# Kernel optimization log

Measured on AMD Instinct MI355X. Metric: run time of the kernel, lower is better.

## Reference

```python
import jax, jax.numpy as jnp
import numpy as np


def setup_inputs() -> dict:
    key = jax.random.key(0)
    k1, k2, k3 = jax.random.split(key, 3)
    N1, N2, P, D = 4, 8, 1024, 128  # P = PH*PW = 32*32 (512px / 16 patch)
    feats = jax.random.normal(k1, (N1, P, D), dtype=jnp.float32)
    nfeats = jax.random.normal(k2, (N2, P, D), dtype=jnp.float32)
    background_masks = jax.random.uniform(k3, (N1, P), dtype=jnp.float32)
    return {"feats": feats, "nfeats": nfeats, "background_masks": background_masks,
            "PH": 32, "PW": 32, "H": 512, "W": 512}


def reference(feats, nfeats, background_masks, PH, PW, H, W):
    # L2-normalize patch embeddings (as in `f / f.norm(dim=-1, keepdim=True)`)
    f = feats / jnp.linalg.norm(feats, axis=-1, keepdims=True)    # [N1,P,D]
    g = nfeats / jnp.linalg.norm(nfeats, axis=-1, keepdims=True)  # [N2,Q,D]
    # Euclidean cdist of unit vectors: d^2 = 2 - 2*dot (clamped at 0)
    dot = jnp.einsum('npd,mqd->nmpq', f, g)                        # [N1,N2,P,Q]
    dist = jnp.sqrt(jnp.maximum(2.0 - 2.0 * dot, 0.0)) / 2.0      # cdist/2, permuted
    # min over normal patches Q -> per-query-patch nearest-neighbor distance
    scores_patch = dist.min(axis=-1)                               # [N1,N2,P]
    scores_patch = scores_patch * background_masks[:, None, :]
    # image score: max over query patches, mean over normal images
    scores = scores_patch.max(axis=-1).mean(axis=-1)               # [N1]
    # pixel map: mean over normal images, reshape to patch grid, bilinear upsample
    sp = scores_patch.mean(axis=1).reshape(-1, PH, PW)             # [N1,PH,PW]
    scores_pixel = jax.image.resize(sp, (sp.shape[0], H, W), method='bilinear')
    return scores, scores_pixel
```

## Files before the change

### kernel.cpp

```cpp
#include <hip/hip_runtime.h>

typedef __attribute__((ext_vector_type(8))) short short8;
typedef __attribute__((ext_vector_type(4))) float f32x4;

typedef const __attribute__((address_space(1))) unsigned int glb_u32;
typedef __attribute__((address_space(3))) unsigned int lds_u32;

static __device__ inline unsigned short f2bf(float x) {
    unsigned int u = __float_as_uint(x);
    u = (u + 0x7FFFu + ((u >> 16) & 1u)) >> 16;
    return (unsigned short)u;
}

__global__ __launch_bounds__(256) void knorm(const float* __restrict__ feats,
                                             const float* __restrict__ nfeats,
                                             unsigned short* __restrict__ fb,
                                             unsigned short* __restrict__ gb) {
    int row = blockIdx.x * 4 + (threadIdx.x >> 6);
    int lane = threadIdx.x & 63;
    const float* src;
    unsigned short* dst;
    if (row < 4096) { src = feats + row * 128;           dst = fb + row * 128; }
    else            { src = nfeats + (row - 4096) * 128; dst = gb + (row - 4096) * 128; }
    float2 v = ((const float2*)src)[lane];
    float ss = v.x * v.x + v.y * v.y;
    #pragma unroll
    for (int d = 32; d; d >>= 1) ss += __shfl_xor(ss, d);
    float inv = 1.0f / sqrtf(ss);
    ushort2 o;
    o.x = f2bf(v.x * inv);
    o.y = f2bf(v.y * inv);
    ((ushort2*)dst)[lane] = o;
}

__global__ __launch_bounds__(512, 4) void kscore(const unsigned short* __restrict__ fb,
                                                 const unsigned short* __restrict__ gb,
                                                 float* __restrict__ sp_part) {
    __shared__ unsigned short gtile[2][64 * 128];
    const int tid = threadIdx.x;
    const int lane = tid & 63;
    const int wave = tid >> 6;
    const int l15 = lane & 15, lhi = lane >> 4;
    const int n = blockIdx.z;
    const int m = blockIdx.y >> 2, qc = blockIdx.y & 3;
    const int pbase = blockIdx.x * 256 + wave * 32;

    short8 a[2][4];
    #pragma unroll
    for (int pg = 0; pg < 2; pg++) {
        const unsigned short* arow = fb + (size_t)(n * 1024 + pbase + pg * 16 + l15) * 128;
        #pragma unroll
        for (int kk = 0; kk < 4; kk++)
            a[pg][kk] = *(const short8*)(arow + kk * 32 + lhi * 8);
    }

    f32x4 mx[2];
    #pragma unroll
    for (int i = 0; i < 4; i++) { mx[0][i] = -1e30f; mx[1][i] = -1e30f; }

    const unsigned short* gBase = gb + ((size_t)m * 1024 + qc * 256) * 128;

    auto stage = [&](int buf, int qb) {
        #pragma unroll
        for (int c = tid; c < 1024; c += 512) {
            int r = c >> 4, s = c & 15;
            int scol = s ^ (r & 7);
            __builtin_amdgcn_global_load_lds(
                (glb_u32*)(gBase + (size_t)(qb + r) * 128 + scol * 8),
                (lds_u32*)((char*)gtile[buf] + c * 16), 16, 0, 0);
        }
    };

    stage(0, 0);
    __syncthreads();
    int buf = 0;
    #pragma unroll
    for (int it = 0; it < 4; it++) {
        if (it < 3) stage(buf ^ 1, (it + 1) * 64);
        const char* tp = (const char*)gtile[buf];
        #pragma unroll
        for (int qt = 0; qt < 4; qt++) {
            int r = qt * 16 + l15;
            int rowoff = r * 256;
            int swz = (r & 7) << 4;
            f32x4 acc0 = {0.f, 0.f, 0.f, 0.f};
            f32x4 acc1 = {0.f, 0.f, 0.f, 0.f};
            #pragma unroll
            for (int kk = 0; kk < 4; kk++) {
                short8 b = *(const short8*)(tp + ((rowoff + kk * 64 + lhi * 16) ^ swz));
                acc0 = __builtin_amdgcn_mfma_f32_16x16x32_bf16(a[0][kk], b, acc0, 0, 0, 0);
                acc1 = __builtin_amdgcn_mfma_f32_16x16x32_bf16(a[1][kk], b, acc1, 0, 0, 0);
            }
            #pragma unroll
            for (int i = 0; i < 4; i++) {
                mx[0][i] = fmaxf(mx[0][i], acc0[i]);
                mx[1][i] = fmaxf(mx[1][i], acc1[i]);
            }
        }
        __syncthreads();
        buf ^= 1;
    }

    #pragma unroll
    for (int pg = 0; pg < 2; pg++)
        #pragma unroll
        for (int i = 0; i < 4; i++) {
            float v = mx[pg][i];
            v = fmaxf(v, __shfl_xor(v, 1));
            v = fmaxf(v, __shfl_xor(v, 2));
            v = fmaxf(v, __shfl_xor(v, 4));
            v = fmaxf(v, __shfl_xor(v, 8));
            mx[pg][i] = v;
        }
    if (l15 == 0) {
        float* dst = sp_part + ((size_t)(n * 8 + m) * 4 + qc) * 1024;
        #pragma unroll
        for (int pg = 0; pg < 2; pg++)
            #pragma unroll
            for (int i = 0; i < 4; i++)
                dst[pbase + pg * 16 + lhi * 4 + i] = mx[pg][i];
    }
}

__global__ __launch_bounds__(256) void kreduce(const float* __restrict__ sp_part,
                                               const float* __restrict__ mask,
                                               float* __restrict__ sp_mean,
                                               float* __restrict__ scores) {
    int n = blockIdx.x, t = threadIdx.x;
    __shared__ float smax[4];
    float sums[4] = {0.f, 0.f, 0.f, 0.f};
    float scoresum = 0.f;
    for (int m = 0; m < 8; m++) {
        const float* base = sp_part + (size_t)(n * 8 + m) * 4 * 1024;
        float lm = -1e30f;
        #pragma unroll
        for (int i = 0; i < 4; i++) {
            int p = i * 256 + t;
            float dot = fmaxf(fmaxf(base[p], base[1024 + p]),
                              fmaxf(base[2048 + p], base[3072 + p]));
            float d = sqrtf(fmaxf(2.0f - 2.0f * dot, 0.0f)) * 0.5f * mask[n * 1024 + p];
            sums[i] += d;
            lm = fmaxf(lm, d);
        }
        #pragma unroll
        for (int d = 32; d; d >>= 1) lm = fmaxf(lm, __shfl_xor(lm, d));
        if ((t & 63) == 0) smax[t >> 6] = lm;
        __syncthreads();
        if (t == 0) scoresum += fmaxf(fmaxf(smax[0], smax[1]), fmaxf(smax[2], smax[3]));
        __syncthreads();
    }
    if (t == 0) scores[n] = scoresum * 0.125f;
    #pragma unroll
    for (int i = 0; i < 4; i++) sp_mean[n * 1024 + i * 256 + t] = sums[i] * 0.125f;
}

__global__ __launch_bounds__(256) void kupsample(const float* __restrict__ sp_mean,
                                                 float* __restrict__ outp) {
    int n = blockIdx.y;
    int idx = blockIdx.x * 256 + threadIdx.x;
    int y = idx >> 9, x = idx & 511;
    float fy = (y + 0.5f) * 0.0625f - 0.5f;
    float fx = (x + 0.5f) * 0.0625f - 0.5f;
    float yf = floorf(fy), xf = floorf(fx);
    float ty = fy - yf, tx = fx - xf;
    int y0 = (int)yf, x0 = (int)xf;
    int y0c = min(max(y0, 0), 31), y1c = min(max(y0 + 1, 0), 31);
    int x0c = min(max(x0, 0), 31), x1c = min(max(x0 + 1, 0), 31);
    const float* s = sp_mean + n * 1024;
    float v00 = s[y0c * 32 + x0c], v01 = s[y0c * 32 + x1c];
    float v10 = s[y1c * 32 + x0c], v11 = s[y1c * 32 + x1c];
    float v0 = v00 + tx * (v01 - v00);
    float v1 = v10 + tx * (v11 - v10);
    outp[(size_t)n * 262144 + idx] = v0 + ty * (v1 - v0);
}

extern "C" void kernel_launch(void* const* d_in, const int* in_sizes, int n_in,
                              void* d_out, int out_size, void* d_ws, size_t ws_size,
                              hipStream_t stream) {
    const float* feats = (const float*)d_in[0];
    const float* nfeats = (const float*)d_in[1];
    const float* mask = (const float*)d_in[2];
    float* out = (float*)d_out;

    unsigned short* fb = (unsigned short*)d_ws;
    unsigned short* gb = fb + 4096 * 128;
    float* sp_part = (float*)((char*)d_ws + 3u * 1024u * 1024u);
    float* sp_mean = sp_part + 4 * 8 * 4 * 1024;

    knorm<<<3072, 256, 0, stream>>>(feats, nfeats, fb, gb);
    kscore<<<dim3(4, 32, 4), 512, 0, stream>>>(fb, gb, sp_part);
    kreduce<<<4, 256, 0, stream>>>(sp_part, mask, sp_mean, out);
    kupsample<<<dim3(1024, 4), 256, 0, stream>>>(sp_mean, out + 4);
}
```

Before: 32.76 us.

## Retile score kernel and fuse reduction with bilinear upsample

```diff
diff --git a/kernel.cpp b/kernel.cpp
--- a/kernel.cpp
+++ b/kernel.cpp
@@ -33,36 +33,38 @@
     ((ushort2*)dst)[lane] = o;
 }
 
-__global__ __launch_bounds__(512, 4) void kscore(const unsigned short* __restrict__ fb,
+__global__ __launch_bounds__(256, 4) void kscore(const unsigned short* __restrict__ fb,
                                                  const unsigned short* __restrict__ gb,
                                                  float* __restrict__ sp_part) {
-    __shared__ unsigned short gtile[2][64 * 128];
+    __shared__ unsigned short gtile[2][32 * 128];
     const int tid = threadIdx.x;
     const int lane = tid & 63;
     const int wave = tid >> 6;
     const int l15 = lane & 15, lhi = lane >> 4;
     const int n = blockIdx.z;
-    const int m = blockIdx.y >> 2, qc = blockIdx.y & 3;
-    const int pbase = blockIdx.x * 256 + wave * 32;
-
-    short8 a[2][4];
-    #pragma unroll
-    for (int pg = 0; pg < 2; pg++) {
+    const int m = blockIdx.y >> 3, qc = blockIdx.y & 7;
+    const int pbase = blockIdx.x * 256 + wave * 64;
+
+    short8 a[4][4];
+    #pragma unroll
+    for (int pg = 0; pg < 4; pg++) {
         const unsigned short* arow = fb + (size_t)(n * 1024 + pbase + pg * 16 + l15) * 128;
         #pragma unroll
         for (int kk = 0; kk < 4; kk++)
             a[pg][kk] = *(const short8*)(arow + kk * 32 + lhi * 8);
     }
 
-    f32x4 mx[2];
-    #pragma unroll
-    for (int i = 0; i < 4; i++) { mx[0][i] = -1e30f; mx[1][i] = -1e30f; }
-
-    const unsigned short* gBase = gb + ((size_t)m * 1024 + qc * 256) * 128;
+    f32x4 mx[4];
+    #pragma unroll
+    for (int pg = 0; pg < 4; pg++)
+        #pragma unroll
+        for (int i = 0; i < 4; i++) mx[pg][i] = -1e30f;
+
+    const unsigned short* gBase = gb + ((size_t)m * 1024 + qc * 128) * 128;
 
     auto stage = [&](int buf, int qb) {
         #pragma unroll
-        for (int c = tid; c < 1024; c += 512) {
+        for (int c = tid; c < 512; c += 256) {
             int r = c >> 4, s = c & 15;
             int scol = s ^ (r & 7);
             __builtin_amdgcn_global_load_lds(
@@ -72,37 +74,43 @@
     };
 
     stage(0, 0);
-    __syncthreads();
-    int buf = 0;
-    #pragma unroll
-    for (int it = 0; it < 4; it++) {
-        if (it < 3) stage(buf ^ 1, (it + 1) * 64);
-        const char* tp = (const char*)gtile[buf];
-        #pragma unroll
-        for (int qt = 0; qt < 4; qt++) {
+    stage(1, 32);
+    #pragma unroll
+    for (int t = 0; t < 4; t++) {
+        if (t < 3) asm volatile("s_waitcnt vmcnt(2)" ::: "memory");
+        else       asm volatile("s_waitcnt vmcnt(0)" ::: "memory");
+        __builtin_amdgcn_s_barrier();
+        __builtin_amdgcn_sched_barrier(0);
+        const char* tp = (const char*)gtile[t & 1];
+        #pragma unroll
+        for (int qt = 0; qt < 2; qt++) {
             int r = qt * 16 + l15;
             int rowoff = r * 256;
             int swz = (r & 7) << 4;
-            f32x4 acc0 = {0.f, 0.f, 0.f, 0.f};
-            f32x4 acc1 = {0.f, 0.f, 0.f, 0.f};
+            f32x4 acc[4];
+            #pragma unroll
+            for (int pg = 0; pg < 4; pg++)
+                #pragma unroll
+                for (int i = 0; i < 4; i++) acc[pg][i] = 0.f;
             #pragma unroll
             for (int kk = 0; kk < 4; kk++) {
                 short8 b = *(const short8*)(tp + ((rowoff + kk * 64 + lhi * 16) ^ swz));
-                acc0 = __builtin_amdgcn_mfma_f32_16x16x32_bf16(a[0][kk], b, acc0, 0, 0, 0);
-                acc1 = __builtin_amdgcn_mfma_f32_16x16x32_bf16(a[1][kk], b, acc1, 0, 0, 0);
+                #pragma unroll
+                for (int pg = 0; pg < 4; pg++)
+                    acc[pg] = __builtin_amdgcn_mfma_f32_16x16x32_bf16(a[pg][kk], b, acc[pg], 0, 0, 0);
             }
             #pragma unroll
-            for (int i = 0; i < 4; i++) {
-                mx[0][i] = fmaxf(mx[0][i], acc0[i]);
-                mx[1][i] = fmaxf(mx[1][i], acc1[i]);
-            }
-        }
-        __syncthreads();
-        buf ^= 1;
-    }
-
-    #pragma unroll
-    for (int pg = 0; pg < 2; pg++)
+            for (int pg = 0; pg < 4; pg++)
+                #pragma unroll
+                for (int i = 0; i < 4; i++) mx[pg][i] = fmaxf(mx[pg][i], acc[pg][i]);
+        }
+        asm volatile("" ::: "memory");
+        __builtin_amdgcn_s_barrier();
+        if (t < 2) stage(t & 1, (t + 2) * 32);
+    }
+
+    #pragma unroll
+    for (int pg = 0; pg < 4; pg++)
         #pragma unroll
         for (int i = 0; i < 4; i++) {
             float v = mx[pg][i];
@@ -113,65 +121,92 @@
             mx[pg][i] = v;
         }
     if (l15 == 0) {
-        float* dst = sp_part + ((size_t)(n * 8 + m) * 4 + qc) * 1024;
-        #pragma unroll
-        for (int pg = 0; pg < 2; pg++)
+        float* dst = sp_part + ((size_t)(n * 8 + m) * 8 + qc) * 1024;
+        #pragma unroll
+        for (int pg = 0; pg < 4; pg++)
             #pragma unroll
             for (int i = 0; i < 4; i++)
                 dst[pbase + pg * 16 + lhi * 4 + i] = mx[pg][i];
     }
 }
 
-__global__ __launch_bounds__(256) void kreduce(const float* __restrict__ sp_part,
-                                               const float* __restrict__ mask,
-                                               float* __restrict__ sp_mean,
-                                               float* __restrict__ scores) {
-    int n = blockIdx.x, t = threadIdx.x;
-    __shared__ float smax[4];
-    float sums[4] = {0.f, 0.f, 0.f, 0.f};
-    float scoresum = 0.f;
-    for (int m = 0; m < 8; m++) {
-        const float* base = sp_part + (size_t)(n * 8 + m) * 4 * 1024;
-        float lm = -1e30f;
-        #pragma unroll
-        for (int i = 0; i < 4; i++) {
-            int p = i * 256 + t;
-            float dot = fmaxf(fmaxf(base[p], base[1024 + p]),
-                              fmaxf(base[2048 + p], base[3072 + p]));
-            float d = sqrtf(fmaxf(2.0f - 2.0f * dot, 0.0f)) * 0.5f * mask[n * 1024 + p];
-            sums[i] += d;
-            lm = fmaxf(lm, d);
-        }
-        #pragma unroll
-        for (int d = 32; d; d >>= 1) lm = fmaxf(lm, __shfl_xor(lm, d));
-        if ((t & 63) == 0) smax[t >> 6] = lm;
-        __syncthreads();
-        if (t == 0) scoresum += fmaxf(fmaxf(smax[0], smax[1]), fmaxf(smax[2], smax[3]));
-        __syncthreads();
-    }
-    if (t == 0) scores[n] = scoresum * 0.125f;
-    #pragma unroll
-    for (int i = 0; i < 4; i++) sp_mean[n * 1024 + i * 256 + t] = sums[i] * 0.125f;
-}
-
-__global__ __launch_bounds__(256) void kupsample(const float* __restrict__ sp_mean,
-                                                 float* __restrict__ outp) {
-    int n = blockIdx.y;
-    int idx = blockIdx.x * 256 + threadIdx.x;
-    int y = idx >> 9, x = idx & 511;
-    float fy = (y + 0.5f) * 0.0625f - 0.5f;
-    float fx = (x + 0.5f) * 0.0625f - 0.5f;
-    float yf = floorf(fy), xf = floorf(fx);
-    float ty = fy - yf, tx = fx - xf;
-    int y0 = (int)yf, x0 = (int)xf;
-    int y0c = min(max(y0, 0), 31), y1c = min(max(y0 + 1, 0), 31);
-    int x0c = min(max(x0, 0), 31), x1c = min(max(x0 + 1, 0), 31);
-    const float* s = sp_mean + n * 1024;
-    float v00 = s[y0c * 32 + x0c], v01 = s[y0c * 32 + x1c];
-    float v10 = s[y1c * 32 + x0c], v11 = s[y1c * 32 + x1c];
-    float v0 = v00 + tx * (v01 - v00);
-    float v1 = v10 + tx * (v11 - v10);
-    outp[(size_t)n * 262144 + idx] = v0 + ty * (v1 - v0);
+__global__ __launch_bounds__(256) void kfinal(const float* __restrict__ sp_part,
+                                              const float* __restrict__ mask,
+                                              float* __restrict__ out) {
+    const int n = blockIdx.y;
+    const int bx = blockIdx.x;
+    const int t = threadIdx.x;
+    float* pix = out + 4;
+
+    if (bx == 64) {
+        __shared__ float smax[4];
+        float acc = 0.f;
+        for (int m = 0; m < 8; m++) {
+            const float* base = sp_part + (size_t)(n * 8 + m) * 8 * 1024;
+            float lm = -1e30f;
+            #pragma unroll
+            for (int i = 0; i < 4; i++) {
+                int p = i * 256 + t;
+                float dot = -1e30f;
+                #pragma unroll
+                for (int qc = 0; qc < 8; qc++) dot = fmaxf(dot, base[qc * 1024 + p]);
+                float d = sqrtf(fmaxf(2.0f - 2.0f * dot, 0.0f)) * 0.5f * mask[n * 1024 + p];
+                lm = fmaxf(lm, d);
+            }
+            #pragma unroll
+            for (int d = 32; d; d >>= 1) lm = fmaxf(lm, __shfl_xor(lm, d));
+            if ((t & 63) == 0) smax[t >> 6] = lm;
+            __syncthreads();
+            if (t == 0) acc += fmaxf(fmaxf(smax[0], smax[1]), fmaxf(smax[2], smax[3]));
+            __syncthreads();
+        }
+        if (t == 0) out[n] = acc * 0.125f;
+        return;
+    }
+
+    __shared__ float sp_row[2][32];
+    const int band = bx * 8;
+    const int pr_lo = (int)floorf((band + 0.5f) * 0.0625f - 0.5f);
+    const int row0 = min(max(pr_lo, 0), 31);
+    const int row1 = min(max(pr_lo + 1, 0), 31);
+    {
+        int v = t >> 2, sub = t & 3;
+        int vr = v >> 5, vc = v & 31;
+        int p = (vr ? row1 : row0) * 32 + vc;
+        float sum = 0.f;
+        #pragma unroll
+        for (int mi = 0; mi < 2; mi++) {
+            int m = sub * 2 + mi;
+            const float* base = sp_part + (size_t)(n * 8 + m) * 8 * 1024 + p;
+            float dot = -1e30f;
+            #pragma unroll
+            for (int qc = 0; qc < 8; qc++) dot = fmaxf(dot, base[qc * 1024]);
+            sum += sqrtf(fmaxf(2.0f - 2.0f * dot, 0.0f)) * 0.5f;
+        }
+        sum *= mask[n * 1024 + p];
+        sum += __shfl_xor(sum, 1);
+        sum += __shfl_xor(sum, 2);
+        if (sub == 0) sp_row[vr][vc] = sum * 0.125f;
+    }
+    __syncthreads();
+    #pragma unroll
+    for (int i = 0; i < 16; i++) {
+        int idx = i * 256 + t;
+        int yl = idx >> 9, x = idx & 511;
+        int y = band + yl;
+        float fy = (y + 0.5f) * 0.0625f - 0.5f;
+        float ty = fy - (float)pr_lo;
+        float fx = (x + 0.5f) * 0.0625f - 0.5f;
+        float xf = floorf(fx);
+        float tx = fx - xf;
+        int x0 = (int)xf;
+        int x0c = min(max(x0, 0), 31), x1c = min(max(x0 + 1, 0), 31);
+        float v00 = sp_row[0][x0c], v01 = sp_row[0][x1c];
+        float v10 = sp_row[1][x0c], v11 = sp_row[1][x1c];
+        float v0 = v00 + tx * (v01 - v00);
+        float v1 = v10 + tx * (v11 - v10);
+        pix[(size_t)n * 262144 + (size_t)y * 512 + x] = v0 + ty * (v1 - v0);
+    }
 }
 
 extern "C" void kernel_launch(void* const* d_in, const int* in_sizes, int n_in,
@@ -185,10 +220,8 @@
     unsigned short* fb = (unsigned short*)d_ws;
     unsigned short* gb = fb + 4096 * 128;
     float* sp_part = (float*)((char*)d_ws + 3u * 1024u * 1024u);
-    float* sp_mean = sp_part + 4 * 8 * 4 * 1024;
 
     knorm<<<3072, 256, 0, stream>>>(feats, nfeats, fb, gb);
-    kscore<<<dim3(4, 32, 4), 512, 0, stream>>>(fb, gb, sp_part);
-    kreduce<<<4, 256, 0, stream>>>(sp_part, mask, sp_mean, out);
-    kupsample<<<dim3(1024, 4), 256, 0, stream>>>(sp_mean, out + 4);
-}
+    kscore<<<dim3(4, 64, 4), 256, 0, stream>>>(fb, gb, sp_part);
+    kfinal<<<dim3(65, 4), 256, 0, stream>>>(sp_part, mask, out);
+}
```

Measured after the change: 59.73 us. 82.3% more time.
